# Optimization experiments

Measured on AMD Instinct MI355X. Metric: run time of the kernel, lower is better.

Reference implementation:

```python
import jax, jax.numpy as jnp
import numpy as np

EMBED = 1024
HEADS = 16
HEAD_DIM = EMBED // HEADS
OUT_DIM = 1024


def setup_inputs() -> dict:
    key = jax.random.key(0)
    ks = jax.random.split(key, 8)
    N, L = 2, 2048
    values = jax.random.normal(ks[0], (N, L, EMBED), dtype=jnp.float32)
    keys_t = jax.random.normal(ks[1], (N, L, EMBED), dtype=jnp.float32)
    query = jax.random.normal(ks[2], (N, L, EMBED), dtype=jnp.float32)
    s = 1.0 / np.sqrt(HEAD_DIM)
    Wv = jax.random.normal(ks[3], (HEAD_DIM, HEAD_DIM), dtype=jnp.float32) * s
    Wk = jax.random.normal(ks[4], (HEAD_DIM, HEAD_DIM), dtype=jnp.float32) * s
    Wq = jax.random.normal(ks[5], (HEAD_DIM, HEAD_DIM), dtype=jnp.float32) * s
    Wout = jax.random.normal(ks[6], (OUT_DIM, EMBED), dtype=jnp.float32) * (1.0 / np.sqrt(EMBED))
    bout = jax.random.normal(ks[7], (OUT_DIM,), dtype=jnp.float32) * 0.01
    return {"values": values, "keys": keys_t, "query": query,
            "Wv": Wv, "Wk": Wk, "Wq": Wq, "Wout": Wout, "bout": bout}


def reference(values, keys, query, Wv, Wk, Wq, Wout, bout):
    N, Lq, _ = query.shape
    Lk = keys.shape[1]
    # split into heads: (N, L, H, D)
    v = values.reshape(N, Lk, HEADS, HEAD_DIM)
    k = keys.reshape(N, Lk, HEADS, HEAD_DIM)
    q = query.reshape(N, Lq, HEADS, HEAD_DIM)
    # per-head shared linear projections (torch Linear: x @ W.T, no bias)
    v = jnp.einsum('nlhd,ed->nlhe', v, Wv)
    k = jnp.einsum('nlhd,ed->nlhe', k, Wk)
    q = jnp.einsum('nqhd,ed->nqhe', q, Wq)
    # scores (N, H, Q, K); NOTE: scale is 1/sqrt(embed_size), per original code
    scores = jnp.einsum('nqhd,nkhd->nhqk', q, k) / jnp.sqrt(jnp.float32(EMBED))
    attn = jax.nn.softmax(scores, axis=-1)
    out = jnp.einsum('nhqk,nkhd->nqhd', attn, v).reshape(N, Lq, EMBED)
    # fc_out: x @ Wout.T + bout
    return out @ Wout.T + bout
```

## Files before the change

kernel.cpp:

```cpp
#include <hip/hip_runtime.h>
#include <cstdint>

typedef __attribute__((ext_vector_type(8))) short short8;
typedef __attribute__((ext_vector_type(4))) float floatx4;
typedef __attribute__((ext_vector_type(4))) _Float16 half4;

#define DEV __device__ __forceinline__

constexpr int NB = 2, Lseq = 2048, NH = 16, HD = 64, EMB = 1024;
constexpr float QSCALE = 0.03125f * 1.4426950408889634f;

DEV uint16_t f2bf(float f) {
  uint32_t x = __builtin_bit_cast(uint32_t, f);
  x += 0x7fffu + ((x >> 16) & 1u);
  return (uint16_t)(x >> 16);
}

DEV uint32_t pack2(float lo, float hi) {
  uint32_t a = __builtin_bit_cast(uint32_t, lo) + 0x8000u;
  uint32_t b = __builtin_bit_cast(uint32_t, hi) + 0x8000u;
  return __builtin_amdgcn_perm(b, a, 0x07060302);
}

DEV uint32_t packh2(float lo, float hi) {
  return __builtin_bit_cast(uint32_t, __builtin_amdgcn_cvt_pkrtz(lo, hi));
}

DEV void gl_lds16(const void* g, void* l) {
  __builtin_amdgcn_global_load_lds((const __attribute__((address_space(1))) void*)g,
                                   (__attribute__((address_space(3))) void*)l, 16, 0, 0);
}

DEV short8 ld8bf(const float* p, float sc) {
  float4 u = *(const float4*)p;
  float4 v = *(const float4*)(p + 4);
  union { short8 s; uint32_t d[4]; } r;
  r.d[0] = pack2(u.x * sc, u.y * sc);
  r.d[1] = pack2(u.z * sc, u.w * sc);
  r.d[2] = pack2(v.x * sc, v.y * sc);
  r.d[3] = pack2(v.z * sc, v.w * sc);
  return r.s;
}

__global__ __launch_bounds__(256) void prep_kernel(
    const float* __restrict__ values, const float* __restrict__ keysrc,
    const float* __restrict__ query, const float* __restrict__ Wv,
    const float* __restrict__ Wk, const float* __restrict__ Wq,
    const float* __restrict__ Wout,
    uint16_t* __restrict__ qp, uint16_t* __restrict__ kp,
    uint16_t* __restrict__ vp, uint16_t* __restrict__ wbf) {
  const int t = threadIdx.x, w = t >> 6, lane = t & 63;
  const int quad = lane >> 4, l16 = lane & 15;
  const int wid = blockIdx.x * 4 + w;
  const int mat = wid >> 10, sub = wid & 1023;

  if (mat == 3) {
#pragma unroll
    for (int i = 0; i < 4; ++i) {
      int idx = sub * 256 + i * 64 + lane;
      float4 v = ((const float4*)Wout)[idx];
      uint2 p;
      p.x = pack2(v.x, v.y);
      p.y = pack2(v.z, v.w);
      ((uint2*)wbf)[idx] = p;
    }
    return;
  }

  floatx4 c[4][4];
#pragma unroll
  for (int i = 0; i < 4; ++i)
#pragma unroll
    for (int j = 0; j < 4; ++j) c[i][j] = floatx4{0.f, 0.f, 0.f, 0.f};

  if (mat < 2) {
    const float* src = mat ? keysrc : query;
    const float* W   = mat ? Wk : Wq;
    const float asc  = mat ? 1.f : QSCALE;
    uint16_t* dst    = mat ? kp : qp;
    const int R0 = sub * 64;
    short8 a[4][2], b[4][2];
#pragma unroll
    for (int dc = 0; dc < 2; ++dc) {
#pragma unroll
      for (int f = 0; f < 4; ++f) {
        a[f][dc] = ld8bf(W + (size_t)(f * 16 + l16) * 64 + dc * 32 + quad * 8, asc);
        b[f][dc] = ld8bf(src + (size_t)(R0 + f * 16 + l16) * 64 + dc * 32 + quad * 8, 1.f);
      }
    }
#pragma unroll
    for (int dc = 0; dc < 2; ++dc)
#pragma unroll
      for (int mf = 0; mf < 4; ++mf)
#pragma unroll
        for (int nf = 0; nf < 4; ++nf)
          c[mf][nf] = __builtin_amdgcn_mfma_f32_16x16x32_bf16(a[mf][dc], b[nf][dc], c[mf][nf], 0, 0, 0);
#pragma unroll
    for (int nf = 0; nf < 4; ++nf) {
      int r = R0 + nf * 16 + l16;
      int h = r & 15, l = (r >> 4) & 2047, n = r >> 15;
      uint16_t* drow = dst + ((size_t)(n * 16 + h) * 2048 + l) * 64;
#pragma unroll
      for (int mf = 0; mf < 4; ++mf) {
        uint2 pk;
        pk.x = pack2(c[mf][nf][0], c[mf][nf][1]);
        pk.y = pack2(c[mf][nf][2], c[mf][nf][3]);
        *(uint2*)(drow + mf * 16 + quad * 4) = pk;
      }
    }
  } else {
    const int nh = sub >> 5, L0 = (sub & 31) * 64;
    const int n = nh >> 4, h = nh & 15;
    short8 a[4][2], b[4][2];
#pragma unroll
    for (int dc = 0; dc < 2; ++dc) {
#pragma unroll
      for (int f = 0; f < 4; ++f) {
        a[f][dc] = ld8bf(values + (size_t)(n * 2048 + L0 + f * 16 + l16) * 1024 + h * 64 + dc * 32 + quad * 8, 1.f);
        b[f][dc] = ld8bf(Wv + (size_t)(f * 16 + l16) * 64 + dc * 32 + quad * 8, 1.f);
      }
    }
#pragma unroll
    for (int dc = 0; dc < 2; ++dc)
#pragma unroll
      for (int mf = 0; mf < 4; ++mf)
#pragma unroll
        for (int nf = 0; nf < 4; ++nf)
          c[mf][nf] = __builtin_amdgcn_mfma_f32_16x16x32_bf16(a[mf][dc], b[nf][dc], c[mf][nf], 0, 0, 0);
#pragma unroll
    for (int nf = 0; nf < 4; ++nf) {
      int d = nf * 16 + l16;
      uint16_t* drow = vp + ((size_t)nh * 64 + d) * 2048 + L0;
#pragma unroll
      for (int mf = 0; mf < 4; ++mf) {
        uint2 pk;
        pk.x = packh2(c[mf][nf][0], c[mf][nf][1]);
        pk.y = packh2(c[mf][nf][2], c[mf][nf][3]);
        *(uint2*)(drow + mf * 16 + quad * 4) = pk;
      }
    }
  }
}

__global__ __launch_bounds__(256, 4) void flash_kernel(const uint16_t* __restrict__ qp,
                                                       const uint16_t* __restrict__ kp,
                                                       const uint16_t* __restrict__ vp,
                                                       float* __restrict__ opart,
                                                       float* __restrict__ psum_g) {
  constexpr int kbn = 16;
  __shared__ uint16_t Kt[2][64 * 64];
  __shared__ uint16_t Vt[2][64 * 64];
  const int t = threadIdx.x;
  const int w = t >> 6, lane = t & 63, quad = lane >> 4, l16 = lane & 15;
  const int nh = blockIdx.x, qt = blockIdx.y, kh = blockIdx.z;
  const int q0 = qt * 128 + w * 32;
  const uint16_t* Qb = qp + (size_t)nh * Lseq * HD;
  const uint16_t* Kb = kp + (size_t)nh * Lseq * HD + (size_t)kh * kbn * 64 * 64;
  const uint16_t* Vb = vp + (size_t)nh * HD * Lseq;
  const int vcol0 = kh * kbn * 64;
  const int srow = lane >> 3, sc8 = (lane & 7) ^ (lane >> 3);

  short8 bq[2][2];
#pragma unroll
  for (int qb = 0; qb < 2; ++qb) {
    bq[qb][0] = *(const short8*)(Qb + (q0 + qb * 16 + l16) * 64 + quad * 8);
    bq[qb][1] = *(const short8*)(Qb + (q0 + qb * 16 + l16) * 64 + 32 + quad * 8);
  }

  floatx4 o[4][2];
  floatx4 lfr[2];
#pragma unroll
  for (int i = 0; i < 4; ++i)
#pragma unroll
    for (int qb = 0; qb < 2; ++qb) o[i][qb] = floatx4{0.f, 0.f, 0.f, 0.f};
  lfr[0] = lfr[1] = floatx4{0.f, 0.f, 0.f, 0.f};
  const _Float16 one = (_Float16)1.0f;
  const half4 vone = {one, one, one, one};

#pragma unroll
  for (int i = 0; i < 2; ++i) {
    int r0 = w * 16 + i * 8;
    gl_lds16(Kb + (r0 + srow) * 64 + sc8 * 8, &Kt[0][r0 * 64]);
    gl_lds16(Vb + (size_t)(r0 + srow) * Lseq + vcol0 + sc8 * 8, &Vt[0][r0 * 64]);
  }

  for (int kb = 0; kb < kbn; ++kb) {
    __syncthreads();
    const int cur = kb & 1;
    if (kb + 1 < kbn) {
      const int nxt = cur ^ 1;
      const uint16_t* kg = Kb + (kb + 1) * (64 * 64);
#pragma unroll
      for (int i = 0; i < 2; ++i) {
        int r0 = w * 16 + i * 8;
        gl_lds16(kg + (r0 + srow) * 64 + sc8 * 8, &Kt[nxt][r0 * 64]);
        gl_lds16(Vb + (size_t)(r0 + srow) * Lseq + vcol0 + (kb + 1) * 64 + sc8 * 8, &Vt[nxt][r0 * 64]);
      }
    }

    floatx4 s[4][2];
#pragma unroll
    for (int kb16 = 0; kb16 < 4; ++kb16)
#pragma unroll
      for (int qb = 0; qb < 2; ++qb) s[kb16][qb] = floatx4{0.f, 0.f, 0.f, 0.f};
#pragma unroll
    for (int dc = 0; dc < 2; ++dc) {
#pragma unroll
      for (int kb16 = 0; kb16 < 4; ++kb16) {
        int row = kb16 * 16 + l16;
        short8 ak = *(const short8*)(&Kt[cur][row * 64 + ((dc * 4 + quad) ^ (row & 7)) * 8]);
        s[kb16][0] = __builtin_amdgcn_mfma_f32_16x16x32_bf16(ak, bq[0][dc], s[kb16][0], 0, 0, 0);
        s[kb16][1] = __builtin_amdgcn_mfma_f32_16x16x32_bf16(ak, bq[1][dc], s[kb16][1], 0, 0, 0);
      }
    }

    half4 bp[4][2];
#pragma unroll
    for (int qb = 0; qb < 2; ++qb) {
#pragma unroll
      for (int kb16 = 0; kb16 < 4; ++kb16) {
        float p0 = __builtin_amdgcn_exp2f(s[kb16][qb][0]);
        float p1 = __builtin_amdgcn_exp2f(s[kb16][qb][1]);
        float p2 = __builtin_amdgcn_exp2f(s[kb16][qb][2]);
        float p3 = __builtin_amdgcn_exp2f(s[kb16][qb][3]);
        union { half4 h4; uint32_t d[2]; } u;
        u.d[0] = packh2(p0, p1);
        u.d[1] = packh2(p2, p3);
        bp[kb16][qb] = u.h4;
      }
    }
#pragma unroll
    for (int kb16 = 0; kb16 < 4; ++kb16) {
      lfr[0] = __builtin_amdgcn_mfma_f32_16x16x16f16(vone, bp[kb16][0], lfr[0], 0, 0, 0);
      lfr[1] = __builtin_amdgcn_mfma_f32_16x16x16f16(vone, bp[kb16][1], lfr[1], 0, 0, 0);
    }

#pragma unroll
    for (int kb16 = 0; kb16 < 4; ++kb16) {
#pragma unroll
      for (int db = 0; db < 4; ++db) {
        int row = db * 16 + l16;
        int ch = (kb16 * 2 + (quad >> 1)) ^ (row & 7);
        half4 av = *(const half4*)(&Vt[cur][row * 64 + ch * 8 + (quad & 1) * 4]);
        o[db][0] = __builtin_amdgcn_mfma_f32_16x16x16f16(av, bp[kb16][0], o[db][0], 0, 0, 0);
        o[db][1] = __builtin_amdgcn_mfma_f32_16x16x16f16(av, bp[kb16][1], o[db][1], 0, 0, 0);
      }
    }
  }

  float* ob = opart + (((size_t)nh * 16 + qt) * 2 + kh) * 8192 + (size_t)w * 8 * 256;
#pragma unroll
  for (int db = 0; db < 4; ++db)
#pragma unroll
    for (int qb = 0; qb < 2; ++qb)
      *(floatx4*)(ob + (db * 2 + qb) * 256 + lane * 4) = o[db][qb];
  if (quad == 0) {
#pragma unroll
    for (int qb = 0; qb < 2; ++qb)
      psum_g[(((size_t)nh * 16 + qt) * 2 + kh) * 128 + w * 32 + qb * 16 + l16] = lfr[qb][0];
  }
}

__global__ __launch_bounds__(256, 2) void gemm_fused64(const float* __restrict__ opart,
                                                       const float* __restrict__ psum_g,
                                                       const uint16_t* __restrict__ Wb,
                                                       const float* __restrict__ bias,
                                                       float* __restrict__ out) {
  __shared__ uint16_t Xt[64 * 64];
  __shared__ uint16_t Wt[2][128 * 64];
  const int t = threadIdx.x, w = t >> 6, lane = t & 63, quad = lane >> 4, l16 = lane & 15;
  const int mblk = blockIdx.x, obk = blockIdx.y;
  const int n = mblk >> 5, qt = (mblk >> 1) & 15, h2 = mblk & 1;
  const int m0 = mblk * 64, o0 = obk * 128;
  const int w_orig = 2 * h2 + (w >> 1), qb = w & 1;
  const int srow = lane >> 3, sc8 = (lane & 7) ^ (lane >> 3);

  floatx4 acc[8];
#pragma unroll
  for (int j = 0; j < 8; ++j) acc[j] = floatx4{0.f, 0.f, 0.f, 0.f};

  floatx4 fa[4], fb[4];
  float la, lb;

  auto issue_loads = [&](int h) {
    size_t tb = ((size_t)(n * 16 + h) * 16 + qt) * 2;
    const float* pa = opart + tb * 8192 + (size_t)w_orig * 2048 + lane * 4;
#pragma unroll
    for (int db = 0; db < 4; ++db) {
      fa[db] = *(const floatx4*)(pa + (db * 2 + qb) * 256);
      fb[db] = *(const floatx4*)(pa + 8192 + (db * 2 + qb) * 256);
    }
    la = psum_g[tb * 128 + w_orig * 32 + qb * 16 + l16];
    lb = psum_g[tb * 128 + 128 + w_orig * 32 + qb * 16 + l16];
  };

  auto pack_write = [&]() {
    float inv = __builtin_amdgcn_rcpf(la + lb);
    int q = w * 16 + l16;
#pragma unroll
    for (int db = 0; db < 4; ++db) {
      float v0 = (fa[db][0] + fb[db][0]) * inv;
      float v1 = (fa[db][1] + fb[db][1]) * inv;
      float v2 = (fa[db][2] + fb[db][2]) * inv;
      float v3 = (fa[db][3] + fb[db][3]) * inv;
      int ch = (db * 2 + (quad >> 1)) ^ (q & 7);
      uint2 pk;
      pk.x = pack2(v0, v1);
      pk.y = pack2(v2, v3);
      *(uint2*)(&Xt[q * 64 + ch * 8 + (quad & 1) * 4]) = pk;
    }
  };

  auto dma_w = [&](int buf, int kt) {
#pragma unroll
    for (int i = 0; i < 4; ++i) {
      int r0 = w * 32 + i * 8;
      gl_lds16(Wb + (size_t)(o0 + r0 + srow) * 1024 + kt * 64 + sc8 * 8, &Wt[buf][r0 * 64]);
    }
  };

  issue_loads(0);
  pack_write();
  dma_w(0, 0);

  for (int kt = 0; kt < 16; ++kt) {
    const int cur = kt & 1;
    __syncthreads();
    if (kt + 1 < 16) {
      issue_loads(kt + 1);
      dma_w(cur ^ 1, kt + 1);
    }
#pragma unroll
    for (int kc = 0; kc < 2; ++kc) {
      int ra = w * 16 + l16;
      short8 a = *(const short8*)(&Xt[ra * 64 + ((kc * 4 + quad) ^ (ra & 7)) * 8]);
#pragma unroll
      for (int nf = 0; nf < 8; ++nf) {
        int rb = nf * 16 + l16;
        short8 b = *(const short8*)(&Wt[cur][rb * 64 + ((kc * 4 + quad) ^ (rb & 7)) * 8]);
        acc[nf] = __builtin_amdgcn_mfma_f32_16x16x32_bf16(a, b, acc[nf], 0, 0, 0);
      }
    }
    if (kt + 1 < 16) pack_write();
  }

#pragma unroll
  for (int nf = 0; nf < 8; ++nf) {
    float bv = bias[o0 + nf * 16 + l16];
#pragma unroll
    for (int r = 0; r < 4; ++r)
      out[(size_t)(m0 + w * 16 + quad * 4 + r) * 1024 + o0 + nf * 16 + l16] = acc[nf][r] + bv;
  }
}

extern "C" void kernel_launch(void* const* d_in, const int* in_sizes, int n_in,
                              void* d_out, int out_size, void* d_ws, size_t ws_size,
                              hipStream_t stream) {
  const float* values = (const float*)d_in[0];
  const float* keys   = (const float*)d_in[1];
  const float* query  = (const float*)d_in[2];
  const float* Wv     = (const float*)d_in[3];
  const float* Wk     = (const float*)d_in[4];
  const float* Wq     = (const float*)d_in[5];
  const float* Wout   = (const float*)d_in[6];
  const float* bout   = (const float*)d_in[7];
  float* out = (float*)d_out;
  (void)ws_size;

  uint16_t* ws  = (uint16_t*)d_ws;
  uint16_t* qp  = ws;
  uint16_t* kp  = ws + (size_t)4194304;
  uint16_t* vp  = ws + (size_t)8388608;
  uint16_t* wbf = ws + (size_t)12582912;
  float* opart  = (float*)(ws + (size_t)13631488);
  float* psum   = opart + (size_t)8388608;

  prep_kernel<<<dim3(1024), dim3(256), 0, stream>>>(values, keys, query, Wv, Wk, Wq, Wout,
                                                    qp, kp, vp, wbf);
  flash_kernel<<<dim3(32, 16, 2), dim3(256), 0, stream>>>(qp, kp, vp, opart, psum);
  gemm_fused64<<<dim3(64, 8), dim3(256), 0, stream>>>(opart, psum, wbf, bout, out);
}
```

Baseline: 178.7 us.

## Drop split-K in flash kernel and emit normalized bf16 attention output

The flash kernel no longer splits the key range into two halves. Each block now walks all 32 key tiles and writes the normalized output directly as bf16 in row-major [N*L, EMB] layout. The output GEMM then streams that bf16 matrix through LDS by DMA instead of reading fp32 partials and row sums and merging them. This removes the fp32 partial traffic and the merge arithmetic, but halves the flash grid to 512 blocks, which may leave the GPU under-occupied. The split-K merge only worked without max subtraction because there is no running max, so it is exact either way.

```diff
diff --git a/kernel.cpp b/kernel.cpp
--- a/kernel.cpp
+++ b/kernel.cpp
@@ -145,19 +145,17 @@
 __global__ __launch_bounds__(256, 4) void flash_kernel(const uint16_t* __restrict__ qp,
                                                        const uint16_t* __restrict__ kp,
                                                        const uint16_t* __restrict__ vp,
-                                                       float* __restrict__ opart,
-                                                       float* __restrict__ psum_g) {
-  constexpr int kbn = 16;
+                                                       uint16_t* __restrict__ xatt) {
+  constexpr int kbn = 32;
   __shared__ uint16_t Kt[2][64 * 64];
   __shared__ uint16_t Vt[2][64 * 64];
   const int t = threadIdx.x;
   const int w = t >> 6, lane = t & 63, quad = lane >> 4, l16 = lane & 15;
-  const int nh = blockIdx.x, qt = blockIdx.y, kh = blockIdx.z;
+  const int nh = blockIdx.x, qt = blockIdx.y;
   const int q0 = qt * 128 + w * 32;
   const uint16_t* Qb = qp + (size_t)nh * Lseq * HD;
-  const uint16_t* Kb = kp + (size_t)nh * Lseq * HD + (size_t)kh * kbn * 64 * 64;
+  const uint16_t* Kb = kp + (size_t)nh * Lseq * HD;
   const uint16_t* Vb = vp + (size_t)nh * HD * Lseq;
-  const int vcol0 = kh * kbn * 64;
   const int srow = lane >> 3, sc8 = (lane & 7) ^ (lane >> 3);
 
   short8 bq[2][2];
@@ -181,7 +179,7 @@
   for (int i = 0; i < 2; ++i) {
     int r0 = w * 16 + i * 8;
     gl_lds16(Kb + (r0 + srow) * 64 + sc8 * 8, &Kt[0][r0 * 64]);
-    gl_lds16(Vb + (size_t)(r0 + srow) * Lseq + vcol0 + sc8 * 8, &Vt[0][r0 * 64]);
+    gl_lds16(Vb + (size_t)(r0 + srow) * Lseq + sc8 * 8, &Vt[0][r0 * 64]);
   }
 
   for (int kb = 0; kb < kbn; ++kb) {
@@ -194,7 +192,7 @@
       for (int i = 0; i < 2; ++i) {
         int r0 = w * 16 + i * 8;
         gl_lds16(kg + (r0 + srow) * 64 + sc8 * 8, &Kt[nxt][r0 * 64]);
-        gl_lds16(Vb + (size_t)(r0 + srow) * Lseq + vcol0 + (kb + 1) * 64 + sc8 * 8, &Vt[nxt][r0 * 64]);
+        gl_lds16(Vb + (size_t)(r0 + srow) * Lseq + (kb + 1) * 64 + sc8 * 8, &Vt[nxt][r0 * 64]);
       }
     }
 
@@ -248,92 +246,59 @@
     }
   }
 
-  float* ob = opart + (((size_t)nh * 16 + qt) * 2 + kh) * 8192 + (size_t)w * 8 * 256;
-#pragma unroll
-  for (int db = 0; db < 4; ++db)
-#pragma unroll
-    for (int qb = 0; qb < 2; ++qb)
-      *(floatx4*)(ob + (db * 2 + qb) * 256 + lane * 4) = o[db][qb];
-  if (quad == 0) {
-#pragma unroll
-    for (int qb = 0; qb < 2; ++qb)
-      psum_g[(((size_t)nh * 16 + qt) * 2 + kh) * 128 + w * 32 + qb * 16 + l16] = lfr[qb][0];
-  }
-}
-
-__global__ __launch_bounds__(256, 2) void gemm_fused64(const float* __restrict__ opart,
-                                                       const float* __restrict__ psum_g,
-                                                       const uint16_t* __restrict__ Wb,
-                                                       const float* __restrict__ bias,
-                                                       float* __restrict__ out) {
-  __shared__ uint16_t Xt[64 * 64];
+  const int n = nh >> 4, h = nh & 15;
+#pragma unroll
+  for (int qb = 0; qb < 2; ++qb) {
+    float inv = __builtin_amdgcn_rcpf(lfr[qb][0]);
+    size_t rowb = (size_t)(n * Lseq + q0 + qb * 16 + l16) * EMB + h * 64;
+#pragma unroll
+    for (int db = 0; db < 4; ++db) {
+      uint2 pk;
+      pk.x = pack2(o[db][qb][0] * inv, o[db][qb][1] * inv);
+      pk.y = pack2(o[db][qb][2] * inv, o[db][qb][3] * inv);
+      *(uint2*)(xatt + rowb + db * 16 + quad * 4) = pk;
+    }
+  }
+}
+
+__global__ __launch_bounds__(256, 2) void gemm_xat(const uint16_t* __restrict__ X,
+                                                   const uint16_t* __restrict__ Wb,
+                                                   const float* __restrict__ bias,
+                                                   float* __restrict__ out) {
+  __shared__ uint16_t Xt[2][64 * 64];
   __shared__ uint16_t Wt[2][128 * 64];
   const int t = threadIdx.x, w = t >> 6, lane = t & 63, quad = lane >> 4, l16 = lane & 15;
-  const int mblk = blockIdx.x, obk = blockIdx.y;
-  const int n = mblk >> 5, qt = (mblk >> 1) & 15, h2 = mblk & 1;
-  const int m0 = mblk * 64, o0 = obk * 128;
-  const int w_orig = 2 * h2 + (w >> 1), qb = w & 1;
+  const int m0 = blockIdx.x * 64, o0 = blockIdx.y * 128;
   const int srow = lane >> 3, sc8 = (lane & 7) ^ (lane >> 3);
 
   floatx4 acc[8];
 #pragma unroll
   for (int j = 0; j < 8; ++j) acc[j] = floatx4{0.f, 0.f, 0.f, 0.f};
 
-  floatx4 fa[4], fb[4];
-  float la, lb;
-
-  auto issue_loads = [&](int h) {
-    size_t tb = ((size_t)(n * 16 + h) * 16 + qt) * 2;
-    const float* pa = opart + tb * 8192 + (size_t)w_orig * 2048 + lane * 4;
-#pragma unroll
-    for (int db = 0; db < 4; ++db) {
-      fa[db] = *(const floatx4*)(pa + (db * 2 + qb) * 256);
-      fb[db] = *(const floatx4*)(pa + 8192 + (db * 2 + qb) * 256);
-    }
-    la = psum_g[tb * 128 + w_orig * 32 + qb * 16 + l16];
-    lb = psum_g[tb * 128 + 128 + w_orig * 32 + qb * 16 + l16];
-  };
-
-  auto pack_write = [&]() {
-    float inv = __builtin_amdgcn_rcpf(la + lb);
-    int q = w * 16 + l16;
-#pragma unroll
-    for (int db = 0; db < 4; ++db) {
-      float v0 = (fa[db][0] + fb[db][0]) * inv;
-      float v1 = (fa[db][1] + fb[db][1]) * inv;
-      float v2 = (fa[db][2] + fb[db][2]) * inv;
-      float v3 = (fa[db][3] + fb[db][3]) * inv;
-      int ch = (db * 2 + (quad >> 1)) ^ (q & 7);
-      uint2 pk;
-      pk.x = pack2(v0, v1);
-      pk.y = pack2(v2, v3);
-      *(uint2*)(&Xt[q * 64 + ch * 8 + (quad & 1) * 4]) = pk;
-    }
-  };
-
-  auto dma_w = [&](int buf, int kt) {
+  auto dma = [&](int buf, int kt) {
+    const int e0 = kt * 64;
+#pragma unroll
+    for (int i = 0; i < 2; ++i) {
+      int r0 = w * 16 + i * 8;
+      gl_lds16(X + (size_t)(m0 + r0 + srow) * 1024 + e0 + sc8 * 8, &Xt[buf][r0 * 64]);
+    }
 #pragma unroll
     for (int i = 0; i < 4; ++i) {
       int r0 = w * 32 + i * 8;
-      gl_lds16(Wb + (size_t)(o0 + r0 + srow) * 1024 + kt * 64 + sc8 * 8, &Wt[buf][r0 * 64]);
+      gl_lds16(Wb + (size_t)(o0 + r0 + srow) * 1024 + e0 + sc8 * 8, &Wt[buf][r0 * 64]);
     }
   };
 
-  issue_loads(0);
-  pack_write();
-  dma_w(0, 0);
+  dma(0, 0);
 
   for (int kt = 0; kt < 16; ++kt) {
     const int cur = kt & 1;
     __syncthreads();
-    if (kt + 1 < 16) {
-      issue_loads(kt + 1);
-      dma_w(cur ^ 1, kt + 1);
-    }
+    if (kt + 1 < 16) dma(cur ^ 1, kt + 1);
 #pragma unroll
     for (int kc = 0; kc < 2; ++kc) {
       int ra = w * 16 + l16;
-      short8 a = *(const short8*)(&Xt[ra * 64 + ((kc * 4 + quad) ^ (ra & 7)) * 8]);
+      short8 a = *(const short8*)(&Xt[cur][ra * 64 + ((kc * 4 + quad) ^ (ra & 7)) * 8]);
 #pragma unroll
       for (int nf = 0; nf < 8; ++nf) {
         int rb = nf * 16 + l16;
@@ -341,7 +306,6 @@
         acc[nf] = __builtin_amdgcn_mfma_f32_16x16x32_bf16(a, b, acc[nf], 0, 0, 0);
       }
     }
-    if (kt + 1 < 16) pack_write();
   }
 
 #pragma unroll
@@ -372,11 +336,10 @@
   uint16_t* kp  = ws + (size_t)4194304;
   uint16_t* vp  = ws + (size_t)8388608;
   uint16_t* wbf = ws + (size_t)12582912;
-  float* opart  = (float*)(ws + (size_t)13631488);
-  float* psum   = opart + (size_t)8388608;
+  uint16_t* xat = ws + (size_t)13631488;
 
   prep_kernel<<<dim3(1024), dim3(256), 0, stream>>>(values, keys, query, Wv, Wk, Wq, Wout,
                                                     qp, kp, vp, wbf);
-  flash_kernel<<<dim3(32, 16, 2), dim3(256), 0, stream>>>(qp, kp, vp, opart, psum);
-  gemm_fused64<<<dim3(64, 8), dim3(256), 0, stream>>>(opart, psum, wbf, bout, out);
-}
+  flash_kernel<<<dim3(32, 16), dim3(256), 0, stream>>>(qp, kp, vp, xat);
+  gemm_xat<<<dim3(64, 8), dim3(256), 0, stream>>>(xat, wbf, bout, out);
+}
```

Result: no change. 181.1 us (+1.3%).
